# Kernel tuning notes

Measured on AMD Instinct MI355X. Metric: run time of the kernel, lower is better.

## Reference

```python
import jax, jax.numpy as jnp
import numpy as np

MAX_SHIFT = 16

def setup_inputs() -> dict:
    key = jax.random.key(0)
    k1, k2 = jax.random.split(key)
    x = jax.random.normal(k1, (64, 3, 512, 512), dtype=jnp.float32)
    # emulate torch: normal(0, sigma=max_shift/2) -> int -> clamp(-max_shift, max_shift)
    shifts = jax.random.randint(k2, (64, 2), -MAX_SHIFT, MAX_SHIFT + 1, dtype=jnp.int32)
    return {"x": x, "shifts": shifts}

def reference(x, shifts):
    # x: [B, C, H, W]; shifts: [B, 2] circular shifts applied to dims (H, W)
    def roll_one(img, s):
        # img: [C, H, W]; roll dims 1 and 2 (H, W), matching torch dims=(1,2)
        return jnp.roll(img, (s[0], s[1]), axis=(1, 2))
    return jax.vmap(roll_one)(x, shifts)
```

## Files before the change

### kernel.cpp

```cpp
#include <hip/hip_runtime.h>

#define BATCH 64
#define CHAN  3
#define HH    512
#define WW    512
#define W4    (WW / 4)

__global__ __launch_bounds__(256) void roll_kernel(
    const float* __restrict__ x,
    const int*   __restrict__ shifts,
    float4*      __restrict__ out)
{
    const int idx = blockIdx.x * blockDim.x + threadIdx.x;
    const int w4 = idx & (W4 - 1);
    const int h  = (idx >> 7) & (HH - 1);
    const int bc = idx >> 16;
    const int b  = bc / 3;

    const int s0 = shifts[2 * b];
    const int s1 = shifts[2 * b + 1];

    const int hs = (h - s0) & (HH - 1);
    const int w0 = (w4 << 2) - s1;

    const float* src = x + ((size_t)bc * HH + hs) * WW;

    float4 v;
    v.x = src[(w0    ) & (WW - 1)];
    v.y = src[(w0 + 1) & (WW - 1)];
    v.z = src[(w0 + 2) & (WW - 1)];
    v.w = src[(w0 + 3) & (WW - 1)];

    out[idx] = v;
}

extern "C" void kernel_launch(void* const* d_in, const int* in_sizes, int n_in,
                              void* d_out, int out_size, void* d_ws, size_t ws_size,
                              hipStream_t stream)
{
    const float* x      = (const float*)d_in[0];
    const int*   shifts = (const int*)d_in[1];
    float4*      out    = (float4*)d_out;

    const int total4 = BATCH * CHAN * HH * W4;
    const int block  = 256;
    const int grid   = total4 / block;

    roll_kernel<<<grid, block, 0, stream>>>(x, shifts, out);
}
```

Measured before the change: 328.8 us.

## Stage source rows in LDS with aligned float4 loads before rotating

Each block now loads two full source rows into shared memory using aligned float4 global loads, then builds each output float4 from two adjacent LDS vectors selected by the column shift. This replaces four unaligned scalar global loads per thread with one vector load. In exchange it adds a block barrier, LDS traffic and a branch on the shift remainder. The kernel is memory-bound, so the previous scalar loads were likely already coalesced through cache.

```diff
diff --git a/kernel.cpp b/kernel.cpp
--- a/kernel.cpp
+++ b/kernel.cpp
@@ -6,45 +6,56 @@
 #define WW    512
 #define W4    (WW / 4)
 
-__global__ __launch_bounds__(256) void roll_kernel(
-    const float* __restrict__ x,
-    const int*   __restrict__ shifts,
-    float4*      __restrict__ out)
+__global__ __launch_bounds__(256) void roll_lds_kernel(
+    const float4* __restrict__ x,
+    const int*    __restrict__ shifts,
+    float4*       __restrict__ out)
 {
-    const int idx = blockIdx.x * blockDim.x + threadIdx.x;
-    const int w4 = idx & (W4 - 1);
-    const int h  = (idx >> 7) & (HH - 1);
-    const int bc = idx >> 16;
-    const int b  = bc / 3;
+    __shared__ float4 lds[2 * W4];
+
+    const int tid    = threadIdx.x;
+    const int r      = tid >> 7;
+    const int w4     = tid & (W4 - 1);
+    const int row_id = blockIdx.x * 2 + r;
+    const int bc     = row_id >> 9;
+    const int h      = row_id & (HH - 1);
+    const int b      = bc / CHAN;
 
     const int s0 = shifts[2 * b];
     const int s1 = shifts[2 * b + 1];
 
     const int hs = (h - s0) & (HH - 1);
-    const int w0 = (w4 << 2) - s1;
+    lds[tid] = x[((size_t)bc * HH + hs) * W4 + w4];
+    __syncthreads();
 
-    const float* src = x + ((size_t)bc * HH + hs) * WW;
+    const int d  = (-s1) & (WW - 1);
+    const int qd = d >> 2;
+    const int rd = d & 3;
+    const int qa = (w4 + qd) & (W4 - 1);
+    const int qb = (qa + 1) & (W4 - 1);
+    const float4 A = lds[(r << 7) + qa];
+    const float4 B = lds[(r << 7) + qb];
 
-    float4 v;
-    v.x = src[(w0    ) & (WW - 1)];
-    v.y = src[(w0 + 1) & (WW - 1)];
-    v.z = src[(w0 + 2) & (WW - 1)];
-    v.w = src[(w0 + 3) & (WW - 1)];
+    float4 o;
+    if      (rd == 0) o = A;
+    else if (rd == 1) o = make_float4(A.y, A.z, A.w, B.x);
+    else if (rd == 2) o = make_float4(A.z, A.w, B.x, B.y);
+    else              o = make_float4(A.w, B.x, B.y, B.z);
 
-    out[idx] = v;
+    out[row_id * W4 + w4] = o;
 }
 
 extern "C" void kernel_launch(void* const* d_in, const int* in_sizes, int n_in,
                               void* d_out, int out_size, void* d_ws, size_t ws_size,
                               hipStream_t stream)
 {
-    const float* x      = (const float*)d_in[0];
-    const int*   shifts = (const int*)d_in[1];
-    float4*      out    = (float4*)d_out;
+    const float4* x      = (const float4*)d_in[0];
+    const int*    shifts = (const int*)d_in[1];
+    float4*       out    = (float4*)d_out;
 
-    const int total4 = BATCH * CHAN * HH * W4;
-    const int block  = 256;
-    const int grid   = total4 / block;
+    const int rows  = BATCH * CHAN * HH;
+    const int grid  = rows / 2;
+    const int block = 256;
 
-    roll_kernel<<<grid, block, 0, stream>>>(x, shifts, out);
+    roll_lds_kernel<<<grid, block, 0, stream>>>(x, shifts, out);
 }
```

After: 316.4 us. 1.04x faster.
